# Optimization experiments

Hardware: AMD Instinct MI355X
Metric: run time of the kernel (lower is better)

## Reference

```python
import jax, jax.numpy as jnp
import numpy as np

B, N, CIN, H, OUT, E = 64, 512, 128, 256, 12, 8192


def setup_inputs() -> dict:
    key = jax.random.key(0)
    ks = jax.random.split(key, 32)
    g = lambda i, shape, s=0.05: jax.random.normal(ks[i], shape, jnp.float32) * s
    inp = {
        "x": jax.random.normal(ks[0], (B, N, CIN), jnp.float32),
        "edge_index": jax.random.randint(ks[1], (2, E), 0, N),
        "edge_weight": jax.random.uniform(ks[2], (E,), dtype=jnp.float32),
    }
    # TGCN2 gate params: GCNConv lin (CIN->H, bias added after aggregation) + Linear(2H->H)
    for j, gate in enumerate(["z", "r", "h"]):
        base = 3 + j * 4
        inp[f"W{gate}"] = g(base, (CIN, H))
        inp[f"b{gate}"] = jnp.zeros((H,), jnp.float32)
        inp[f"l{gate}_W"] = g(base + 1, (2 * H, H))
        inp[f"l{gate}_b"] = jnp.zeros((H,), jnp.float32)
    # 2-layer GRU (torch layout: W_ih [3H,in], W_hh [3H,H]); eval mode (dropout off)
    inp["Wih0"] = g(16, (3 * H, CIN)); inp["Whh0"] = g(17, (3 * H, H))
    inp["bih0"] = jnp.zeros((3 * H,), jnp.float32); inp["bhh0"] = jnp.zeros((3 * H,), jnp.float32)
    inp["Wih1"] = g(18, (3 * H, H)); inp["Whh1"] = g(19, (3 * H, H))
    inp["bih1"] = jnp.zeros((3 * H,), jnp.float32); inp["bhh1"] = jnp.zeros((3 * H,), jnp.float32)
    # heads (stored as [in,out] so y = x @ W + b, matching torch x @ W.T + b)
    inp["l1_W"] = g(20, (H, 1)); inp["l1_b"] = jnp.zeros((1,), jnp.float32)
    inp["l2_W"] = g(21, (H, 1)); inp["l2_b"] = jnp.zeros((1,), jnp.float32)
    inp["l3_W"] = g(22, (2, OUT)); inp["l3_b"] = jnp.zeros((OUT,), jnp.float32)
    return inp


def _gcn_norm(edge_index, edge_weight, n_nodes):
    # improved=True -> self loops with fill value 2.0; sym normalization
    loop = jnp.arange(n_nodes)
    src = jnp.concatenate([edge_index[0], loop])
    tgt = jnp.concatenate([edge_index[1], loop])
    ew = jnp.concatenate([edge_weight, jnp.full((n_nodes,), 2.0, edge_weight.dtype)])
    deg = jax.ops.segment_sum(ew, tgt, num_segments=n_nodes)
    dinv = jnp.where(deg > 0, deg ** -0.5, 0.0)
    return src, tgt, dinv[src] * ew * dinv[tgt]


def _gcn_conv(x, W, b, src, tgt, norm):
    xw = x @ W                                   # [B,N,H]
    msg = xw[:, src, :] * norm[None, :, None]    # gather from sources [B,E+N,H]
    out = jnp.zeros_like(xw).at[:, tgt, :].add(msg)  # scatter-add to targets
    return out + b


def _gru_layer(x_sbf, Wih, Whh, bih, bhh):
    h_dim = Whh.shape[1]
    h0 = jnp.zeros((x_sbf.shape[1], h_dim), x_sbf.dtype)

    def step(h, xt):
        gi = xt @ Wih.T + bih
        gh = h @ Whh.T + bhh
        ir, iz, inn = jnp.split(gi, 3, axis=-1)
        hr, hz, hn = jnp.split(gh, 3, axis=-1)
        r = jax.nn.sigmoid(ir + hr)
        z = jax.nn.sigmoid(iz + hz)
        n = jnp.tanh(inn + r * hn)
        h_new = (1.0 - z) * n + z * h
        return h_new, h_new

    _, ys = jax.lax.scan(step, h0, x_sbf)
    return ys  # [S,B,H]


def reference(x, edge_index, edge_weight, Wz, bz, lz_W, lz_b, Wr, br, lr_W, lr_b,
              Wh, bh, lh_W, lh_b, Wih0, Whh0, bih0, bhh0, Wih1, Whh1, bih1, bhh1,
              l1_W, l1_b, l2_W, l2_b, l3_W, l3_b):
    n_nodes = x.shape[1]
    # GRU branch (node dim treated as sequence, as in the source)
    xs = jnp.transpose(x, (1, 0, 2))             # [N,B,CIN]
    h1 = _gru_layer(xs, Wih0, Whh0, bih0, bhh0)
    h2 = _gru_layer(h1, Wih1, Whh1, bih1, bhh1)
    temp = jnp.transpose(h2, (1, 0, 2))          # [B,N,H]
    gru_out = temp @ l2_W + l2_b                 # [B,N,1]
    # TGCN2 cell with H0 = 0
    src, tgt, norm = _gcn_norm(edge_index, edge_weight, n_nodes)
    Hst = jnp.zeros((x.shape[0], n_nodes, lz_W.shape[1]), x.dtype)
    cz = _gcn_conv(x, Wz, bz, src, tgt, norm)
    Z = jax.nn.sigmoid(jnp.concatenate([cz, Hst], axis=2) @ lz_W + lz_b)
    cr = _gcn_conv(x, Wr, br, src, tgt, norm)
    R = jax.nn.sigmoid(jnp.concatenate([cr, Hst], axis=2) @ lr_W + lr_b)
    ch = _gcn_conv(x, Wh, bh, src, tgt, norm)
    H_tilde = jnp.tanh(jnp.concatenate([ch, Hst * R], axis=2) @ lh_W + lh_b)
    Hn = Z * Hst + (1.0 - Z) * H_tilde           # [B,N,H]
    h = jax.nn.relu(Hn) @ l1_W + l1_b            # [B,N,1]
    cat = jnp.concatenate([gru_out, h], axis=2)  # [B,N,2]
    return cat @ l3_W + l3_b                     # [B,N,OUT]
```

## Files before the change

### kernel.cpp

```cpp
#include <hip/hip_runtime.h>


typedef unsigned short u16;
typedef unsigned long long u64;
typedef short s8v __attribute__((ext_vector_type(8)));
typedef float f4v __attribute__((ext_vector_type(4)));

#define NBATCH 64
#define NNODE  512
#define DCIN   128
#define DHID   256
#define NEDGE  8192
#define RING   8
#define SLOTU16 16384

__device__ __forceinline__ u16 f2b(float f) {
    union { float f; unsigned int i; } v; v.f = f;
    unsigned int x = v.i;
    return (u16)((x + 0x7FFFu + ((x >> 16) & 1u)) >> 16);
}
__device__ __forceinline__ float sigm(float x)  { return 1.0f / (1.0f + __expf(-x)); }
__device__ __forceinline__ float tanh_(float x) { return 1.0f - 2.0f / (1.0f + __expf(2.0f * x)); }
__device__ __forceinline__ f4v mfma16(s8v a, s8v b, f4v c) {
    return __builtin_amdgcn_mfma_f32_16x16x32_bf16(a, b, c, 0, 0, 0);
}
__device__ __forceinline__ s8v ld_ring(const u64* p) {
    union { u64 d[2]; s8v v; } u;
    u.d[0] = __hip_atomic_load(p,     __ATOMIC_RELAXED, __HIP_MEMORY_SCOPE_AGENT);
    u.d[1] = __hip_atomic_load(p + 1, __ATOMIC_RELAXED, __HIP_MEMORY_SCOPE_AGENT);
    return u.v;
}
__device__ __forceinline__ void st_ring(u64* p, s8v v) {
    union { s8v v; u64 d[2]; } u; u.v = v;
    __hip_atomic_store(p,     u.d[0], __ATOMIC_RELAXED, __HIP_MEMORY_SCOPE_AGENT);
    __hip_atomic_store(p + 1, u.d[1], __ATOMIC_RELAXED, __HIP_MEMORY_SCOPE_AGENT);
}
__device__ __forceinline__ void wait_stamp(const int* sp, int tgt, int l) {
    while (true) {
        int v = 0x7fffffff;
        if (l < 16) v = __hip_atomic_load(sp + l, __ATOMIC_RELAXED, __HIP_MEMORY_SCOPE_AGENT);
        if (__all(v >= tgt)) break;
        __builtin_amdgcn_s_sleep(2);
    }
    asm volatile("" ::: "memory");
}
__device__ __forceinline__ void wait_stamp_slack(const int* sp, int tgt,
                                                 const int* fp, int tgtf, int l) {
    while (true) {
        int v = 0x7fffffff, tg = -0x7fffffff;
        if (l < 16)      { v = __hip_atomic_load(sp + l, __ATOMIC_RELAXED, __HIP_MEMORY_SCOPE_AGENT); tg = tgt; }
        else if (l < 32) { v = __hip_atomic_load(fp + (l - 16), __ATOMIC_RELAXED, __HIP_MEMORY_SCOPE_AGENT); tg = tgtf; }
        if (__all(v >= tg)) break;
        __builtin_amdgcn_s_sleep(2);
    }
    asm volatile("" ::: "memory");
}
__device__ __forceinline__ s8v cvt8(const float* p) {
    s8v r;
    #pragma unroll
    for (int e = 0; e < 8; ++e) r[e] = (short)f2b(p[e]);
    return r;
}

__global__ void init_kernel(float* deg, int* counts, int* syncb) {
    int i = blockIdx.x * blockDim.x + threadIdx.x;
    if (i < NNODE) { deg[i] = 2.0f; counts[i] = 1; }
    if (i < 2048) syncb[i] = 0;
}

__global__ void edge_deg_kernel(const int* __restrict__ ei, const float* __restrict__ ew,
                                float* deg, int* counts) {
    int e = blockIdx.x * blockDim.x + threadIdx.x;
    if (e < NEDGE) {
        int t = ei[NEDGE + e];
        atomicAdd(&deg[t], ew[e]);
        atomicAdd(&counts[t], 1);
    }
}

__global__ void scan_kernel(const float* __restrict__ deg, const int* __restrict__ counts,
                            float* __restrict__ dinv, int* __restrict__ rowptr,
                            int* __restrict__ cursor, int* __restrict__ col,
                            float* __restrict__ val) {
    __shared__ int sc[NNODE];
    int i = threadIdx.x;
    float d = deg[i];
    float di = (d > 0.0f) ? (1.0f / sqrtf(d)) : 0.0f;
    dinv[i] = di;
    int cnt = counts[i];
    sc[i] = cnt;
    __syncthreads();
    for (int ofs = 1; ofs < NNODE; ofs <<= 1) {
        int add = (i >= ofs) ? sc[i - ofs] : 0;
        __syncthreads();
        sc[i] += add;
        __syncthreads();
    }
    int ex = sc[i] - cnt;
    rowptr[i] = ex;
    if (i == NNODE - 1) rowptr[NNODE] = sc[NNODE - 1];
    col[ex] = i;
    val[ex] = di * 2.0f * di;
    cursor[i] = ex + 1;
}

__global__ void fill_kernel(const int* __restrict__ ei, const float* __restrict__ ew,
                            const float* __restrict__ dinv, int* cursor,
                            int* __restrict__ col, float* __restrict__ val) {
    int e = blockIdx.x * blockDim.x + threadIdx.x;
    if (e < NEDGE) {
        int s = ei[e], t = ei[NEDGE + e];
        int p = atomicAdd(&cursor[t], 1);
        col[p] = s;
        val[p] = dinv[s] * ew[e] * dinv[t];
    }
}

__global__ void fold_kernel(const float* __restrict__ Wz, const float* __restrict__ lzW,
                            const float* __restrict__ bz, const float* __restrict__ lzb,
                            const float* __restrict__ Wh, const float* __restrict__ lhW,
                            const float* __restrict__ bh, const float* __restrict__ lhb,
                            u16* __restrict__ Wf, float* __restrict__ bfold) {
    int nidx = blockIdx.x;
    int g = nidx & 1, j = nidx >> 1;
    int k = threadIdx.x;
    const float* W = g ? Wh : Wz;
    const float* L = g ? lhW : lzW;
    float acc = 0.0f;
    for (int m = 0; m < DHID; ++m)
        acc += W[k * DHID + m] * L[m * DHID + j];
    Wf[nidx * DCIN + k] = f2b(acc);
    if (k == 0) {
        const float* bg = g ? bh : bz;
        const float* lb = g ? lhb : lzb;
        float ab = 0.0f;
        for (int m = 0; m < DHID; ++m) ab += bg[m] * L[m * DHID + j];
        bfold[nidx] = ab + lb[j];
    }
}

__global__ void repack_w_kernel(const float* __restrict__ Wih, const float* __restrict__ Whh,
                                int KCX, int KC, int KX, int KH, u16* __restrict__ dst) {
    int id = blockIdx.x * 256 + threadIdx.x;
    int total = 16 * KC * 3 * 64;
    if (id >= total) return;
    int l = id & 63; int rest = id >> 6;
    int g = rest % 3; rest /= 3;
    int kc = rest % KC; rest /= KC;
    int r = rest;
    int j = r * 16 + (l & 15);
    int q = l >> 4;
    const float* src; int k;
    if (kc < KCX) { src = Wih + (size_t)(g * 256 + j) * KX; k = kc * 32 + q * 8; }
    else          { src = Whh + (size_t)(g * 256 + j) * KH; k = (kc - KCX) * 32 + q * 8; }
    u16* d = dst + (((size_t)(r * KC + kc)) * 3 + g) * 512 + l * 8;
    #pragma unroll
    for (int e = 0; e < 8; ++e) d[e] = f2b(src[k + e]);
}

__global__ __launch_bounds__(256)
void tgcn_kernel(const float* __restrict__ x, const int* __restrict__ rowptr,
                 const int* __restrict__ col, const float* __restrict__ val,
                 const u16* __restrict__ Wf, const float* __restrict__ bfold,
                 const float* __restrict__ l1W, float* __restrict__ hdot) {
    __shared__ u16 As[64][136];
    const int tid = threadIdx.x;
    const int bx = blockIdx.x;
    const int b = bx >> 3;
    const int n0 = (bx & 7) * 64;
    {
        const int c = tid & 127;
        const int half = tid >> 7;
        for (int it = 0; it < 32; ++it) {
            int r = it * 2 + half;
            int n = n0 + r;
            int s = rowptr[n], e = rowptr[n + 1];
            float acc = 0.0f;
            for (int i = s; i < e; ++i)
                acc += val[i] * x[((size_t)b * NNODE + col[i]) * DCIN + c];
            As[r][c] = f2b(acc);
        }
    }
    __syncthreads();
    const int w = tid >> 6, l = tid & 63;
    const int ncol = l & 15, q = l >> 4, ko = q * 8;
    s8v af[4];
    #pragma unroll
    for (int kc = 0; kc < 4; ++kc)
        af[kc] = *(const s8v*)(&As[w * 16 + ncol][kc * 32 + ko]);
    float partial[4] = {0.f, 0.f, 0.f, 0.f};
    for (int nc = 0; nc < 32; ++nc) {
        int n = nc * 16 + ncol;
        const u16* brow = Wf + (size_t)n * DCIN + ko;
        f4v acc = {0.f, 0.f, 0.f, 0.f};
        #pragma unroll
        for (int kc = 0; kc < 4; ++kc)
            acc = mfma16(af[kc], *(const s8v*)(brow + kc * 32), acc);
        float bias = bfold[n];
        float l1w = l1W[n >> 1];
        #pragma unroll
        for (int rr = 0; rr < 4; ++rr) {
            float v = acc[rr] + bias;
            float o = __shfl_xor(v, 1);
            float zpre = (ncol & 1) ? o : v;
            float hpre = (ncol & 1) ? v : o;
            float hn = (1.0f - sigm(zpre)) * tanh_(hpre);
            hn = hn > 0.0f ? hn : 0.0f;
            if (!(ncol & 1)) partial[rr] += hn * l1w;
        }
    }
    #pragma unroll
    for (int rr = 0; rr < 4; ++rr) {
        float p = partial[rr];
        p += __shfl_xor(p, 1); p += __shfl_xor(p, 2);
        p += __shfl_xor(p, 4); p += __shfl_xor(p, 8);
        if (ncol == 0)
            hdot[bx * 64 + w * 16 + q * 4 + rr] = p;
    }
}

__global__ __launch_bounds__(256)
void gru_pipe_kernel(const float* __restrict__ x,
                     const u16* __restrict__ Wpk0, const u16* __restrict__ Wpk1,
                     const float* __restrict__ bih0, const float* __restrict__ bhh0,
                     const float* __restrict__ bih1, const float* __restrict__ bhh1,
                     const float* __restrict__ l2W,
                     u16* __restrict__ h0ring, u16* __restrict__ h1ring,
                     int* syncb, float* __restrict__ gpartg) {
    __shared__ u16 wlds[16 * 3 * 512];
    __shared__ u16 tile[4][16][16];

    const int tid = threadIdx.x;
    const int w = tid >> 6;
    const int l = tid & 63;
    const int q = l >> 4, ncol = l & 15;
    const bool isL1 = blockIdx.x >= 16;
    const int rblk = blockIdx.x & 15;
    const int KC = isL1 ? 16 : 12;

    int* fL1 = syncb + 16;
    int* st0 = syncb + 64;
    int* st1 = syncb + 64 + 512;

    {
        const s8v* src = (const s8v*)((isL1 ? Wpk1 : Wpk0) + (size_t)rblk * KC * 3 * 512);
        s8v* dst = (s8v*)wlds;
        for (int i = tid; i < KC * 3 * 64; i += 256) dst[i] = src[i];
    }
    const int j = rblk * 16 + ncol;
    const float* bihp = isL1 ? bih1 : bih0;
    const float* bhhp = isL1 ? bhh1 : bhh0;
    const float br = bihp[j] + bhhp[j];
    const float bz = bihp[256 + j] + bhhp[256 + j];
    const float bi = bihp[512 + j];
    const float bhn = bhhp[512 + j];
    const float l2v = isL1 ? l2W[j] : 0.0f;
    float hreg[4] = {0.f, 0.f, 0.f, 0.f};
    const int qbase = 2 * (rblk & 1);
    u16* myring = isL1 ? h1ring : h0ring;
    int* myst = isL1 ? st1 : st0;
    int* myflag = (isL1 ? fL1 : syncb) + rblk;
    const s8v* wf = (const s8v*)wlds;
    const float* xrow = x + ((size_t)(w * 16 + ncol) * NNODE) * DCIN + q * 8;
    __syncthreads();

    for (int t = 0; t < NNODE; ++t) {
        const int scur = t & (RING - 1), sprev = (t - 1) & (RING - 1);
        f4v accR = {0,0,0,0}, accZ = {0,0,0,0}, accNi = {0,0,0,0}, accNh = {0,0,0,0};
        if (!isL1) {
            const float* xp = xrow + (size_t)t * DCIN;
            #pragma unroll
            for (int kc = 0; kc < 4; ++kc) {
                s8v a = cvt8(xp + kc * 32);
                accR  = mfma16(a, wf[(kc * 3 + 0) * 64 + l], accR);
                accZ  = mfma16(a, wf[(kc * 3 + 1) * 64 + l], accZ);
                accNi = mfma16(a, wf[(kc * 3 + 2) * 64 + l], accNi);
            }
            if (t > 0) {
                wait_stamp_slack(st0 + sprev * 64 + w * 16, t, fL1, t - 7, l);
                const u64* s1 = (const u64*)(h0ring + (size_t)sprev * SLOTU16);
                s8v a1[8];
                #pragma unroll
                for (int k = 0; k < 8; ++k)
                    a1[k] = ld_ring(s1 + (size_t)(w * 8 + k) * 128 + l * 2);
                #pragma unroll
                for (int k = 0; k < 8; ++k) {
                    int kc = 4 + k;
                    accR  = mfma16(a1[k], wf[(kc * 3 + 0) * 64 + l], accR);
                    accZ  = mfma16(a1[k], wf[(kc * 3 + 1) * 64 + l], accZ);
                    accNh = mfma16(a1[k], wf[(kc * 3 + 2) * 64 + l], accNh);
                }
            }
        } else {
            wait_stamp(st0 + scur * 64 + w * 16, t + 1, l);
            const u64* s0 = (const u64*)(h0ring + (size_t)scur * SLOTU16);
            s8v a0[8];
            #pragma unroll
            for (int k = 0; k < 8; ++k)
                a0[k] = ld_ring(s0 + (size_t)(w * 8 + k) * 128 + l * 2);
            #pragma unroll
            for (int k = 0; k < 8; ++k) {
                accR  = mfma16(a0[k], wf[(k * 3 + 0) * 64 + l], accR);
                accZ  = mfma16(a0[k], wf[(k * 3 + 1) * 64 + l], accZ);
                accNi = mfma16(a0[k], wf[(k * 3 + 2) * 64 + l], accNi);
            }
            if (t > 0) {
                wait_stamp(st1 + sprev * 64 + w * 16, t, l);
                const u64* s1 = (const u64*)(h1ring + (size_t)sprev * SLOTU16);
                s8v a1[8];
                #pragma unroll
                for (int k = 0; k < 8; ++k)
                    a1[k] = ld_ring(s1 + (size_t)(w * 8 + k) * 128 + l * 2);
                #pragma unroll
                for (int k = 0; k < 8; ++k) {
                    int kc = 8 + k;
                    accR  = mfma16(a1[k], wf[(kc * 3 + 0) * 64 + l], accR);
                    accZ  = mfma16(a1[k], wf[(kc * 3 + 1) * 64 + l], accZ);
                    accNh = mfma16(a1[k], wf[(kc * 3 + 2) * 64 + l], accNh);
                }
            }
        }
        float pd[4];
        #pragma unroll
        for (int rr = 0; rr < 4; ++rr) {
            float rv = sigm(accR[rr] + br);
            float zv = sigm(accZ[rr] + bz);
            float nv = tanh_(accNi[rr] + bi + rv * (accNh[rr] + bhn));
            float hn = nv + zv * (hreg[rr] - nv);
            hreg[rr] = hn;
            tile[w][q * 4 + rr][ncol] = f2b(hn);
            pd[rr] = hn * l2v;
        }
        if (q == qbase || q == qbase + 1) {
            s8v v = *(const s8v*)&tile[w][ncol][8 * (q - qbase)];
            u64* dst = (u64*)(myring + (size_t)scur * SLOTU16)
                       + (size_t)(w * 8 + (rblk >> 1)) * 128 + l * 2;
            st_ring(dst, v);
        }
        asm volatile("s_waitcnt vmcnt(0)" ::: "memory");
        if (l == 0)
            __hip_atomic_store(myst + scur * 64 + w * 16 + rblk, t + 1,
                               __ATOMIC_RELAXED, __HIP_MEMORY_SCOPE_AGENT);
        if (isL1) {
            #pragma unroll
            for (int rr = 0; rr < 4; ++rr) {
                float v = pd[rr];
                v += __shfl_xor(v, 1); v += __shfl_xor(v, 2);
                v += __shfl_xor(v, 4); v += __shfl_xor(v, 8);
                if (ncol == 0)
                    gpartg[((size_t)t * 16 + rblk) * 64 + w * 16 + q * 4 + rr] = v;
            }
        }
        __syncthreads();
        if (tid == 0)
            __hip_atomic_store(myflag, t + 1,
                               __ATOMIC_RELAXED, __HIP_MEMORY_SCOPE_AGENT);
    }
}

__global__ __launch_bounds__(256)
void head_kernel(const float* __restrict__ gpartg, const float* __restrict__ hdot,
                 const float* __restrict__ l1b, const float* __restrict__ l2b,
                 const float* __restrict__ l3W, const float* __restrict__ l3b,
                 float* __restrict__ out) {
    int idx = blockIdx.x * 256 + threadIdx.x;
    if (idx >= NBATCH * NNODE * 12) return;
    int r = idx / 12, oc = idx - r * 12;
    int b = r >> 9, n = r & 511;
    float g = 0.0f;
    #pragma unroll
    for (int k = 0; k < 16; ++k) g += gpartg[((size_t)n * 16 + k) * 64 + b];
    g += l2b[0];
    float hh = hdot[r] + l1b[0];
    out[idx] = g * l3W[oc] + hh * l3W[12 + oc] + l3b[oc];
}

static hipStream_t g_side = nullptr;
static hipEvent_t  g_evA  = nullptr;
static hipEvent_t  g_evB  = nullptr;
namespace {
struct SideInit {
    SideInit() {
        if (hipStreamCreateWithFlags(&g_side, hipStreamNonBlocking) != hipSuccess) g_side = nullptr;
        if (hipEventCreateWithFlags(&g_evA, hipEventDisableTiming) != hipSuccess) g_evA = nullptr;
        if (hipEventCreateWithFlags(&g_evB, hipEventDisableTiming) != hipSuccess) g_evB = nullptr;
    }
};
static SideInit g_side_init;
}

extern "C" void kernel_launch(void* const* d_in, const int* in_sizes, int n_in,
                              void* d_out, int out_size, void* d_ws, size_t ws_size,
                              hipStream_t stream) {
    const float* x    = (const float*)d_in[0];
    const int*   ei   = (const int*)  d_in[1];
    const float* ew   = (const float*)d_in[2];
    const float* Wz   = (const float*)d_in[3];
    const float* bz   = (const float*)d_in[4];
    const float* lzW  = (const float*)d_in[5];
    const float* lzb  = (const float*)d_in[6];
    const float* Wh   = (const float*)d_in[11];
    const float* bh   = (const float*)d_in[12];
    const float* lhW  = (const float*)d_in[13];
    const float* lhb  = (const float*)d_in[14];
    const float* Wih0 = (const float*)d_in[15];
    const float* Whh0 = (const float*)d_in[16];
    const float* bih0 = (const float*)d_in[17];
    const float* bhh0 = (const float*)d_in[18];
    const float* Wih1 = (const float*)d_in[19];
    const float* Whh1 = (const float*)d_in[20];
    const float* bih1 = (const float*)d_in[21];
    const float* bhh1 = (const float*)d_in[22];
    const float* l1W  = (const float*)d_in[23];
    const float* l1b  = (const float*)d_in[24];
    const float* l2W  = (const float*)d_in[25];
    const float* l2b  = (const float*)d_in[26];
    const float* l3W  = (const float*)d_in[27];
    const float* l3b  = (const float*)d_in[28];

    char* ws = (char*)d_ws;
    size_t o = 0;
    auto take = [&](size_t nbytes) {
        char* p = ws + o;
        o = (o + nbytes + 255) & ~(size_t)255;
        return p;
    };
    float* deg    = (float*)take(NNODE * 4);
    float* dinv   = (float*)take(NNODE * 4);
    int*   rowptr = (int*)  take((NNODE + 1) * 4);
    int*   cursor = (int*)  take(NNODE * 4);
    int*   col    = (int*)  take((NEDGE + NNODE) * 4);
    float* val    = (float*)take((NEDGE + NNODE) * 4);
    u16*   Wf     = (u16*)  take((size_t)512 * DCIN * 2);
    float* bfold  = (float*)take(512 * 4);
    float* hdot   = (float*)take((size_t)NBATCH * NNODE * 4);
    float* gpartg = (float*)take((size_t)NNODE * 16 * 64 * 4);
    u16*   Wpk0   = (u16*)  take((size_t)16 * 12 * 3 * 512 * 2);
    u16*   Wpk1   = (u16*)  take((size_t)16 * 16 * 3 * 512 * 2);
    u16*   h0ring = (u16*)  take((size_t)RING * SLOTU16 * 2);
    u16*   h1ring = (u16*)  take((size_t)RING * SLOTU16 * 2);
    int*   syncb  = (int*)  take(8192);
    if (o > ws_size) return;

    const bool fork = (g_side && g_evA && g_evB);
    hipStream_t sideS = fork ? g_side : stream;

    init_kernel<<<8, 256, 0, stream>>>(deg, cursor, syncb);

    if (fork) {
        hipEventRecord(g_evA, stream);
        hipStreamWaitEvent(sideS, g_evA, 0);
    }

    edge_deg_kernel<<<NEDGE / 256, 256, 0, sideS>>>(ei, ew, deg, cursor);
    scan_kernel<<<1, NNODE, 0, sideS>>>(deg, cursor, dinv, rowptr, cursor, col, val);
    fill_kernel<<<NEDGE / 256, 256, 0, sideS>>>(ei, ew, dinv, cursor, col, val);
    fold_kernel<<<512, DCIN, 0, sideS>>>(Wz, lzW, bz, lzb, Wh, lhW, bh, lhb, Wf, bfold);
    tgcn_kernel<<<512, 256, 0, sideS>>>(x, rowptr, col, val, Wf, bfold, l1W, hdot);
    if (fork) hipEventRecord(g_evB, sideS);

    repack_w_kernel<<<(16 * 12 * 3 * 64 + 255) / 256, 256, 0, stream>>>(
        Wih0, Whh0, 4, 12, DCIN, DHID, Wpk0);
    repack_w_kernel<<<(16 * 16 * 3 * 64 + 255) / 256, 256, 0, stream>>>(
        Wih1, Whh1, 8, 16, DHID, DHID, Wpk1);
    gru_pipe_kernel<<<32, 256, 0, stream>>>(x, Wpk0, Wpk1, bih0, bhh0,
                                            bih1, bhh1, l2W, h0ring, h1ring,
                                            syncb, gpartg);

    if (fork) hipStreamWaitEvent(stream, g_evB, 0);
    head_kernel<<<(NBATCH * NNODE * 12 + 255) / 256, 256, 0, stream>>>(
        gpartg, hdot, l1b, l2b, l3W, l3b, (float*)d_out);
    (void)in_sizes; (void)n_in; (void)out_size;
}
```

Baseline: 2.281 ms.

## Prefetch next-step x rows and layer-0 hidden state in GRU recurrence

Layer-0 blocks now load the next timestep's x inputs into registers after publishing the current step, so the global load latency overlaps the barrier and the next wait. Layer-1 blocks opportunistically prefetch the next h0 ring slot when its stamps are already ready. They also load h1 before consuming h0, reordering the dependency waits. The spin-wait sleep is shortened to react faster. This adds register pressure and more polling traffic in exchange for hiding load latency on the serial critical path.

```diff
diff --git a/kernel.cpp b/kernel.cpp
--- a/kernel.cpp
+++ b/kernel.cpp
@@ -40,7 +40,7 @@
         int v = 0x7fffffff;
         if (l < 16) v = __hip_atomic_load(sp + l, __ATOMIC_RELAXED, __HIP_MEMORY_SCOPE_AGENT);
         if (__all(v >= tgt)) break;
-        __builtin_amdgcn_s_sleep(2);
+        __builtin_amdgcn_s_sleep(1);
     }
     asm volatile("" ::: "memory");
 }
@@ -51,7 +51,7 @@
         if (l < 16)      { v = __hip_atomic_load(sp + l, __ATOMIC_RELAXED, __HIP_MEMORY_SCOPE_AGENT); tg = tgt; }
         else if (l < 32) { v = __hip_atomic_load(fp + (l - 16), __ATOMIC_RELAXED, __HIP_MEMORY_SCOPE_AGENT); tg = tgtf; }
         if (__all(v >= tg)) break;
-        __builtin_amdgcn_s_sleep(2);
+        __builtin_amdgcn_s_sleep(1);
     }
     asm volatile("" ::: "memory");
 }
@@ -262,16 +262,28 @@
     int* myflag = (isL1 ? fL1 : syncb) + rblk;
     const s8v* wf = (const s8v*)wlds;
     const float* xrow = x + ((size_t)(w * 16 + ncol) * NNODE) * DCIN + q * 8;
+
+    float xraw[32];
+    s8v a0p[8];
+    bool pf = false;
+    if (!isL1) {
+        #pragma unroll
+        for (int i = 0; i < 32; ++i)
+            xraw[i] = xrow[(i >> 3) * 32 + (i & 7)];
+    }
     __syncthreads();
 
     for (int t = 0; t < NNODE; ++t) {
         const int scur = t & (RING - 1), sprev = (t - 1) & (RING - 1);
+        const int snxt = (t + 1) & (RING - 1);
         f4v accR = {0,0,0,0}, accZ = {0,0,0,0}, accNi = {0,0,0,0}, accNh = {0,0,0,0};
+        int pv = 0x7fffffff;
         if (!isL1) {
-            const float* xp = xrow + (size_t)t * DCIN;
             #pragma unroll
             for (int kc = 0; kc < 4; ++kc) {
-                s8v a = cvt8(xp + kc * 32);
+                s8v a;
+                #pragma unroll
+                for (int e = 0; e < 8; ++e) a[e] = (short)f2b(xraw[kc * 8 + e]);
                 accR  = mfma16(a, wf[(kc * 3 + 0) * 64 + l], accR);
                 accZ  = mfma16(a, wf[(kc * 3 + 1) * 64 + l], accZ);
                 accNi = mfma16(a, wf[(kc * 3 + 2) * 64 + l], accNi);
@@ -292,25 +304,31 @@
                 }
             }
         } else {
-            wait_stamp(st0 + scur * 64 + w * 16, t + 1, l);
-            const u64* s0 = (const u64*)(h0ring + (size_t)scur * SLOTU16);
-            s8v a0[8];
-            #pragma unroll
-            for (int k = 0; k < 8; ++k)
-                a0[k] = ld_ring(s0 + (size_t)(w * 8 + k) * 128 + l * 2);
-            #pragma unroll
-            for (int k = 0; k < 8; ++k) {
-                accR  = mfma16(a0[k], wf[(k * 3 + 0) * 64 + l], accR);
-                accZ  = mfma16(a0[k], wf[(k * 3 + 1) * 64 + l], accZ);
-                accNi = mfma16(a0[k], wf[(k * 3 + 2) * 64 + l], accNi);
-            }
+            s8v a1[8];
             if (t > 0) {
                 wait_stamp(st1 + sprev * 64 + w * 16, t, l);
                 const u64* s1 = (const u64*)(h1ring + (size_t)sprev * SLOTU16);
-                s8v a1[8];
                 #pragma unroll
                 for (int k = 0; k < 8; ++k)
                     a1[k] = ld_ring(s1 + (size_t)(w * 8 + k) * 128 + l * 2);
+            }
+            if (t + 1 < NNODE && l < 16)
+                pv = __hip_atomic_load(st0 + snxt * 64 + w * 16 + l,
+                                       __ATOMIC_RELAXED, __HIP_MEMORY_SCOPE_AGENT);
+            if (!pf) {
+                wait_stamp(st0 + scur * 64 + w * 16, t + 1, l);
+                const u64* s0 = (const u64*)(h0ring + (size_t)scur * SLOTU16);
+                #pragma unroll
+                for (int k = 0; k < 8; ++k)
+                    a0p[k] = ld_ring(s0 + (size_t)(w * 8 + k) * 128 + l * 2);
+            }
+            #pragma unroll
+            for (int k = 0; k < 8; ++k) {
+                accR  = mfma16(a0p[k], wf[(k * 3 + 0) * 64 + l], accR);
+                accZ  = mfma16(a0p[k], wf[(k * 3 + 1) * 64 + l], accZ);
+                accNi = mfma16(a0p[k], wf[(k * 3 + 2) * 64 + l], accNi);
+            }
+            if (t > 0) {
                 #pragma unroll
                 for (int k = 0; k < 8; ++k) {
                     int kc = 8 + k;
@@ -341,7 +359,22 @@
         if (l == 0)
             __hip_atomic_store(myst + scur * 64 + w * 16 + rblk, t + 1,
                                __ATOMIC_RELAXED, __HIP_MEMORY_SCOPE_AGENT);
-        if (isL1) {
+        if (!isL1) {
+            if (t + 1 < NNODE) {
+                const float* xp = xrow + (size_t)(t + 1) * DCIN;
+                #pragma unroll
+                for (int i = 0; i < 32; ++i)
+                    xraw[i] = xp[(i >> 3) * 32 + (i & 7)];
+            }
+        } else {
+            pf = false;
+            if (t + 1 < NNODE && __all(pv >= t + 2)) {
+                const u64* s0 = (const u64*)(h0ring + (size_t)snxt * SLOTU16);
+                #pragma unroll
+                for (int k = 0; k < 8; ++k)
+                    a0p[k] = ld_ring(s0 + (size_t)(w * 8 + k) * 128 + l * 2);
+                pf = true;
+            }
             #pragma unroll
             for (int rr = 0; rr < 4; ++rr) {
                 float v = pd[rr];
```

Result: slower. 2.334 ms (+2.3%).
